# Kernel tuning notes

Measured on AMD Instinct MI355X. Metric: run time of the kernel, lower is better.

## Reference

```python
import jax, jax.numpy as jnp
import numpy as np

N_HEAD = 16

def setup_inputs() -> dict:
    key = jax.random.key(0)
    k1, k2, k3, k4, k5 = jax.random.split(key, 5)
    B, S, D = 2, 2048, 1024
    return {
        "hidden_states": jax.random.normal(k1, (B, S, D), jnp.float32),
        "w_attn": jax.random.normal(k2, (D, 3 * D), jnp.float32) * 0.02,
        "b_attn": jax.random.normal(k3, (3 * D,), jnp.float32) * 0.02,
        "w_proj": jax.random.normal(k4, (D, D), jnp.float32) * 0.02,
        "b_proj": jax.random.normal(k5, (D,), jnp.float32) * 0.02,
    }

def reference(hidden_states, w_attn, b_attn, w_proj, b_proj):
    B, S, D = hidden_states.shape
    H = N_HEAD
    Dh = D // H
    qkv = hidden_states @ w_attn + b_attn              # [B,S,3D]
    q, k, v = jnp.split(qkv, 3, axis=-1)
    def split_heads(x):
        return x.reshape(B, S, H, Dh).transpose(0, 2, 1, 3)  # [B,H,S,Dh]
    q, k, v = split_heads(q), split_heads(k), split_heads(v)
    # scale=True: divide by sqrt(head_dim) (v.size(-1))
    scores = jnp.einsum("bhqd,bhkd->bhqk", q, k) / jnp.sqrt(jnp.float32(Dh))
    attn = jax.nn.softmax(scores, axis=-1)             # [B,H,S,S]
    out = jnp.einsum("bhqk,bhkd->bhqd", attn, v)       # [B,H,S,Dh]
    out = out.transpose(0, 2, 1, 3).reshape(B, S, D)   # merge heads
    return out @ w_proj + b_proj
```

## Files before the change

kernel.cpp:

```cpp
#include <hip/hip_runtime.h>
#include <hip/hip_bf16.h>

typedef __attribute__((ext_vector_type(8))) short bf16x8;
typedef __attribute__((ext_vector_type(4))) float f32x4;
typedef __attribute__((ext_vector_type(16))) float f32x16;

#define LOG2E 1.4426950408889634f
#define SCALE_F (0.125f * LOG2E)

__device__ inline unsigned short f2bf(float f) {
  union { float f; unsigned u; } x; x.f = f;
  unsigned u = x.u;
  unsigned r = u + 0x7FFFu + ((u >> 16) & 1u);
  return (unsigned short)(r >> 16);
}

__device__ inline unsigned cvtpk(float lo, float hi) {
  unsigned r;
  asm("v_cvt_pk_bf16_f32 %0, %1, %2" : "=v"(r) : "v"(lo), "v"(hi));
  return r;
}

__device__ inline void gload16(const unsigned short* g, unsigned short* l) {
  __builtin_amdgcn_global_load_lds(
      (const __attribute__((address_space(1))) unsigned int*)g,
      (__attribute__((address_space(3))) unsigned int*)l, 16, 0, 0);
}

template <int J>
__device__ inline bf16x8 pack_pfrag(f32x16 p) {
  int X, Y, Z, W;
  asm("v_cvt_pk_bf16_f32 %0, %1, %2" : "=v"(X) : "v"(p[J + 0]), "v"(p[J + 1]));
  asm("v_cvt_pk_bf16_f32 %0, %1, %2" : "=v"(Y) : "v"(p[J + 2]), "v"(p[J + 3]));
  asm("v_cvt_pk_bf16_f32 %0, %1, %2" : "=v"(Z) : "v"(p[J + 4]), "v"(p[J + 5]));
  asm("v_cvt_pk_bf16_f32 %0, %1, %2" : "=v"(W) : "v"(p[J + 6]), "v"(p[J + 7]));
  asm("v_permlane32_swap_b32 %0, %1" : "+v"(X), "+v"(Z));
  asm("v_permlane32_swap_b32 %0, %1" : "+v"(Y), "+v"(W));
  union { int w[4]; bf16x8 v; } u;
  u.w[0] = X; u.w[1] = Y; u.w[2] = Z; u.w[3] = W;
  return u.v;
}

__global__ __launch_bounds__(256) void cvt_bf16(const float* __restrict__ X,
                                                unsigned short* __restrict__ Y, int n4) {
  int i = blockIdx.x * blockDim.x + threadIdx.x;
  int stride = gridDim.x * blockDim.x;
  for (; i < n4; i += stride) {
    float4 v = reinterpret_cast<const float4*>(X)[i];
    ushort4 o;
    o.x = f2bf(v.x); o.y = f2bf(v.y); o.z = f2bf(v.z); o.w = f2bf(v.w);
    reinterpret_cast<ushort4*>(Y)[i] = o;
  }
}

__global__ __launch_bounds__(256) void transpose_cvt(const float* __restrict__ W,
                                                     unsigned short* __restrict__ WT,
                                                     int K, int N) {
  __shared__ unsigned short Tl[64][72];
  const int t = threadIdx.x;
  const int n0 = blockIdx.x * 64, k0 = blockIdx.y * 64;
#pragma unroll
  for (int i = 0; i < 4; ++i) {
    int idx = t + i * 256;
    int r = idx >> 4, c4 = (idx & 15) << 2;
    float4 v = *reinterpret_cast<const float4*>(&W[(size_t)(k0 + r) * N + n0 + c4]);
    Tl[c4 + 0][r] = f2bf(v.x);
    Tl[c4 + 1][r] = f2bf(v.y);
    Tl[c4 + 2][r] = f2bf(v.z);
    Tl[c4 + 3][r] = f2bf(v.w);
  }
  __syncthreads();
#pragma unroll
  for (int i = 0; i < 2; ++i) {
    int idx = t + i * 256;
    int rr = idx >> 3, cc = (idx & 7) << 3;
    *reinterpret_cast<int4*>(&WT[(size_t)(n0 + rr) * K + k0 + cc]) =
        *reinterpret_cast<const int4*>(&Tl[rr][cc]);
  }
}

__global__ __launch_bounds__(512, 2) void gemm_qkv_8p(
    const unsigned short* __restrict__ A, const unsigned short* __restrict__ Bt,
    const float* __restrict__ bias,
    unsigned short* __restrict__ qw, unsigned short* __restrict__ kw,
    unsigned short* __restrict__ vtg) {
  __shared__ unsigned short Abuf[2][16384];
  __shared__ unsigned short Bbuf[2][12288];
  const int t = threadIdx.x, lane = t & 63, wid = t >> 6;
  const int wm = wid >> 2, wn = wid & 3;
  const int orig = blockIdx.x;
  const int nid = (orig & 7) * 32 + (orig >> 3);
  const int mt = nid >> 4, nt = nid & 15;
  const int row0 = mt * 256, col0 = nt * 192;
  const int lr = lane & 15, kq = lane >> 4;
  const int srow_lo = lane >> 3;
  const int scg = (lane & 7) ^ srow_lo;
  const unsigned short* Ab = A + (size_t)row0 * 1024;
  const unsigned short* Bb = Bt + (size_t)col0 * 1024;
  f32x4 acc[8][3] = {};

#define SA8(bs, kt)                                                              \
  {                                                                              \
    const unsigned short* Ap = Ab + (kt) * 64;                                   \
    _Pragma("unroll") for (int i = 0; i < 4; ++i) {                              \
      int g = wid * 4 + i;                                                       \
      int rrel = g * 8 + srow_lo;                                                \
      gload16(&Ap[(size_t)rrel * 1024 + scg * 8], &Abuf[bs][g * 512]);           \
    }                                                                            \
  }
#define SB8(bs, kt)                                                              \
  {                                                                              \
    const unsigned short* Bp = Bb + (kt) * 64;                                   \
    _Pragma("unroll") for (int i = 0; i < 3; ++i) {                              \
      int g = wid * 3 + i;                                                       \
      int rrel = g * 8 + srow_lo;                                                \
      gload16(&Bp[(size_t)rrel * 1024 + scg * 8], &Bbuf[bs][g * 512]);           \
    }                                                                            \
  }
#define RDA(dst, mh)                                                             \
  _Pragma("unroll") for (int m = 0; m < 4; ++m)                                  \
  _Pragma("unroll") for (int ks = 0; ks < 2; ++ks) {                             \
    int row = wm * 128 + (mh) * 64 + m * 16 + lr;                                \
    dst[m][ks] = *reinterpret_cast<const bf16x8*>(                               \
        &Ac[row * 64 + (((ks * 4 + kq) ^ (row & 7)) << 3)]);                     \
  }
#define RDB2(dst)                                                                \
  _Pragma("unroll") for (int n = 0; n < 2; ++n)                                  \
  _Pragma("unroll") for (int ks = 0; ks < 2; ++ks) {                             \
    int row = wn * 48 + n * 16 + lr;                                             \
    dst[n][ks] = *reinterpret_cast<const bf16x8*>(                               \
        &Bc[row * 64 + (((ks * 4 + kq) ^ (row & 7)) << 3)]);                     \
  }
#define RDB1(dst)                                                                \
  _Pragma("unroll") for (int ks = 0; ks < 2; ++ks) {                             \
    int row = wn * 48 + 32 + lr;                                                 \
    dst[0][ks] = *reinterpret_cast<const bf16x8*>(                               \
        &Bc[row * 64 + (((ks * 4 + kq) ^ (row & 7)) << 3)]);                     \
  }
#define QMM2(mh, afv, bfv)                                                       \
  _Pragma("unroll") for (int m = 0; m < 4; ++m)                                  \
  _Pragma("unroll") for (int n = 0; n < 2; ++n)                                  \
  _Pragma("unroll") for (int ks = 0; ks < 2; ++ks)                               \
    acc[(mh) * 4 + m][n] = __builtin_amdgcn_mfma_f32_16x16x32_bf16(              \
        afv[m][ks], bfv[n][ks], acc[(mh) * 4 + m][n], 0, 0, 0);
#define QMM1(mh, afv, bfv)                                                       \
  _Pragma("unroll") for (int m = 0; m < 4; ++m)                                  \
  _Pragma("unroll") for (int ks = 0; ks < 2; ++ks)                               \
    acc[(mh) * 4 + m][2] = __builtin_amdgcn_mfma_f32_16x16x32_bf16(              \
        afv[m][ks], bfv[0][ks], acc[(mh) * 4 + m][2], 0, 0, 0);
#define BAR8 __builtin_amdgcn_s_barrier();

  SA8(0, 0) SB8(0, 0)
  asm volatile("s_waitcnt vmcnt(0)" ::: "memory");
  BAR8
  __builtin_amdgcn_sched_barrier(0);

  for (int kt = 0; kt < 16; ++kt) {
    const int buf = kt & 1;
    const unsigned short* Ac = Abuf[buf];
    const unsigned short* Bc = Bbuf[buf];
    bf16x8 af0[4][2], af1[4][2], bf0[2][2], bf1[1][2];
    RDA(af0, 0) RDB2(bf0)
    if (kt < 15) SA8(buf ^ 1, kt + 1)
    BAR8
    __builtin_amdgcn_s_setprio(1); QMM2(0, af0, bf0) __builtin_amdgcn_s_setprio(0);
    BAR8
    RDA(af1, 1)
    if (kt < 15) SB8(buf ^ 1, kt + 1)
    BAR8
    __builtin_amdgcn_s_setprio(1); QMM2(1, af1, bf0) __builtin_amdgcn_s_setprio(0);
    BAR8
    RDB1(bf1)
    BAR8
    __builtin_amdgcn_s_setprio(1); QMM1(0, af0, bf1) __builtin_amdgcn_s_setprio(0);
    BAR8
    if (kt < 15) { asm volatile("s_waitcnt vmcnt(0)" ::: "memory"); }
    BAR8
    __builtin_amdgcn_s_setprio(1); QMM1(1, af1, bf1) __builtin_amdgcn_s_setprio(0);
    BAR8
    __builtin_amdgcn_sched_barrier(0);
  }
#undef SA8
#undef SB8
#undef RDA
#undef RDB2
#undef RDB1
#undef QMM2
#undef QMM1
#undef BAR8

  const int rbase = (lane >> 4) * 4;
#pragma unroll
  for (int mm = 0; mm < 8; ++mm) {
#pragma unroll
    for (int nn = 0; nn < 3; ++nn) {
      int c = col0 + wn * 48 + nn * 16 + lr;
      int which = c >> 10;
      int d = c & 1023;
      int h = d >> 6, dh = d & 63;
      float bv = bias[c];
      int m0 = row0 + wm * 128 + mm * 16 + rbase;
      int b = m0 >> 11, s0 = m0 & 2047;
      if (which == 2) {
        int kt = s0 >> 6, key0 = s0 & 63;
        ushort4 pv;
        pv.x = f2bf(acc[mm][nn][0] + bv);
        pv.y = f2bf(acc[mm][nn][1] + bv);
        pv.z = f2bf(acc[mm][nn][2] + bv);
        pv.w = f2bf(acc[mm][nn][3] + bv);
        *reinterpret_cast<ushort4*>(
            &vtg[(((size_t)(b * 16 + h) * 32 + kt) * 64 + dh) * 64 + key0]) = pv;
      } else if (which == 1) {
#pragma unroll
        for (int r = 0; r < 4; ++r)
          kw[(((size_t)b * 16 + h) * 2048 + (s0 + r)) * 64 + dh] = f2bf(acc[mm][nn][r] + bv);
      } else {
#pragma unroll
        for (int r = 0; r < 4; ++r)
          qw[(((size_t)b * 16 + h) * 2048 + (s0 + r)) * 64 + dh] =
              f2bf((acc[mm][nn][r] + bv) * SCALE_F);
      }
    }
  }
}

#define GST(bs, kt)                                                             \
  {                                                                             \
    const unsigned short* Ap = Ab + (kt) * 32;                                  \
    const unsigned short* Bp = Bb + (kt) * 32;                                  \
    _Pragma("unroll") for (int i = 0; i < 2; ++i) {                             \
      int row = i * 64 + wid * 16 + s_r;                                        \
      gload16(&Ap[(size_t)row * 1024 + s_c], &Al[bs][i * 2048 + wid * 512]);    \
      gload16(&Bp[(size_t)row * 1024 + s_c], &Bl[bs][i * 2048 + wid * 512]);    \
    }                                                                           \
  }

#define GBODY(br)                                                               \
  {                                                                             \
    bf16x8 af[4], bfv[4];                                                       \
    _Pragma("unroll") for (int mm = 0; mm < 4; ++mm) {                          \
      int row = wr + mm * 16 + lr;                                              \
      af[mm] = *reinterpret_cast<const bf16x8*>(                                \
          &Al[br][row * 32 + ((kq ^ (lr & 3)) << 3)]);                          \
    }                                                                           \
    _Pragma("unroll") for (int nn = 0; nn < 4; ++nn) {                          \
      int row = wc + nn * 16 + lr;                                              \
      bfv[nn] = *reinterpret_cast<const bf16x8*>(                               \
          &Bl[br][row * 32 + ((kq ^ (lr & 3)) << 3)]);                          \
    }                                                                           \
    _Pragma("unroll") for (int mm = 0; mm < 4; ++mm)                            \
      _Pragma("unroll") for (int nn = 0; nn < 4; ++nn)                          \
        acc[mm][nn] =                                                           \
            __builtin_amdgcn_mfma_f32_16x16x32_bf16(af[mm], bfv[nn],            \
                                                    acc[mm][nn], 0, 0, 0);      \
  }

#define VMC4 asm volatile("s_waitcnt vmcnt(4)" ::: "memory");
#define VMC0 asm volatile("s_waitcnt vmcnt(0)" ::: "memory");
#define BAR __builtin_amdgcn_s_barrier();

__global__ __launch_bounds__(256) void gemm_proj_b(
    const unsigned short* __restrict__ A, const unsigned short* __restrict__ Bt,
    const float* __restrict__ bias, float* __restrict__ out) {
  const int N = 1024;
  __shared__ unsigned short Al[3][4096];
  __shared__ unsigned short Bl[3][4096];
  const int t = threadIdx.x, lane = t & 63, wid = t >> 6;
  const int wr = (wid >> 1) * 64, wc = (wid & 1) * 64;
  const int orig = blockIdx.x + 8 * blockIdx.y;
  const int nid = (orig & 7) * 32 + (orig >> 3);
  const int row0 = (nid >> 3) * 128, col0 = (nid & 7) * 128;
  const int lr = lane & 15, kq = lane >> 4;
  const int s_r = lane >> 2;
  const int s_c = ((lane & 3) ^ (s_r & 3)) * 8;
  const unsigned short* Ab = A + (size_t)row0 * 1024;
  const unsigned short* Bb = Bt + (size_t)col0 * 1024;
  f32x4 acc[4][4] = {};

  GST(0, 0) GST(1, 1)
  VMC4 BAR
  for (int tt = 0; tt < 30; tt += 3) {
    GST(2, tt + 2) GBODY(0) VMC4 BAR
    GST(0, tt + 3) GBODY(1) VMC4 BAR
    GST(1, tt + 4) GBODY(2) VMC4 BAR
  }
  GBODY(0) VMC0 BAR
  GBODY(1)

  const int rbase = (lane >> 4) * 4;
#pragma unroll
  for (int mm = 0; mm < 4; ++mm) {
#pragma unroll
    for (int nn = 0; nn < 4; ++nn) {
      int c = col0 + wc + nn * 16 + lr;
      float bv = bias[c];
#pragma unroll
      for (int r = 0; r < 4; ++r) {
        int m = row0 + wr + mm * 16 + rbase + r;
        out[(size_t)m * N + c] = acc[mm][nn][r] + bv;
      }
    }
  }
}

__global__ __launch_bounds__(512, 4) void attn_kernel(
    const unsigned short* __restrict__ qw, const unsigned short* __restrict__ kw,
    const unsigned short* __restrict__ vtg, unsigned short* __restrict__ ow) {
  __shared__ char smem[65536];
  unsigned short* KV = (unsigned short*)smem;
  unsigned short* Ol = (unsigned short*)smem;
  float* EX = (float*)(smem + 18432);
  const int t = threadIdx.x, lane = t & 63, wid = t >> 6;
  const int half = wid >> 2, wq = wid & 3;
  const int l31 = lane & 31, hi = lane >> 5;
  const int orig = blockIdx.x + 16 * blockIdx.y;
  const int nid = (orig & 7) * 64 + (orig >> 3);
  const int qt = nid & 15, bh = nid >> 4;
  const int b = bh >> 4, h = bh & 15;
  const unsigned short* Qg = qw + (size_t)bh * 2048 * 64;
  const unsigned short* Kg = kw + (size_t)bh * 2048 * 64;
  const unsigned short* Vg = vtg + (size_t)bh * 32 * 4096;
  const int q0 = qt * 128 + wq * 32;

  union { short s[8]; bf16x8 v; } one_u;
#pragma unroll
  for (int i = 0; i < 8; ++i) one_u.s[i] = (short)0x3F80;
  const bf16x8 ones = one_u.v;

  bf16x8 qf[4];
#pragma unroll
  for (int kc = 0; kc < 4; ++kc)
    qf[kc] = *reinterpret_cast<const bf16x8*>(&Qg[(q0 + l31) * 64 + kc * 16 + hi * 8]);

  f32x16 oA = {0,0,0,0,0,0,0,0,0,0,0,0,0,0,0,0};
  f32x16 oB = {0,0,0,0,0,0,0,0,0,0,0,0,0,0,0,0};
  f32x16 lC = {0,0,0,0,0,0,0,0,0,0,0,0,0,0,0,0};

  const int srow_lo = lane >> 3;
  const int scg = (lane & 7) ^ srow_lo;

#define STAGE(buf, kt)                                                              \
  {                                                                                 \
    const unsigned short* Kt = Kg + (size_t)(kt) * 4096;                            \
    const unsigned short* Vs = Vg + (size_t)(kt) * 4096;                            \
    unsigned short* Kl = KV + half * 16384 + (buf) * 8192;                          \
    unsigned short* Vl = Kl + 4096;                                                 \
    _Pragma("unroll") for (int i = 0; i < 2; ++i) {                                 \
      int chunk = wq * 2 + i;                                                       \
      int row = chunk * 8 + srow_lo;                                                \
      gload16(&Kt[row * 64 + scg * 8], &Kl[chunk * 512]);                           \
      gload16(&Vs[row * 64 + scg * 8], &Vl[chunk * 512]);                           \
    }                                                                               \
  }

  const int kt0 = half * 16;
  STAGE(0, kt0)

  for (int it = 0; it < 16; ++it) {
    const int cur = it & 1;
    if (it + 1 < 16) {
      STAGE(cur ^ 1, kt0 + it + 1)
      asm volatile("s_waitcnt vmcnt(4)" ::: "memory");
    } else {
      asm volatile("s_waitcnt vmcnt(0)" ::: "memory");
    }
    __builtin_amdgcn_s_barrier();
    const unsigned short* Kl = KV + half * 16384 + cur * 8192;
    const unsigned short* Vl = Kl + 4096;

    f32x16 sA = {0,0,0,0,0,0,0,0,0,0,0,0,0,0,0,0};
    f32x16 sB = {0,0,0,0,0,0,0,0,0,0,0,0,0,0,0,0};
    __builtin_amdgcn_s_setprio(1);
#pragma unroll
    for (int kc = 0; kc < 4; ++kc) {
      bf16x8 k0f = *reinterpret_cast<const bf16x8*>(
          &Kl[l31 * 64 + (((kc * 2 + hi) ^ (l31 & 7)) << 3)]);
      bf16x8 k1f = *reinterpret_cast<const bf16x8*>(
          &Kl[(32 + l31) * 64 + (((kc * 2 + hi) ^ (l31 & 7)) << 3)]);
      sA = __builtin_amdgcn_mfma_f32_32x32x16_bf16(k0f, qf[kc], sA, 0, 0, 0);
      sB = __builtin_amdgcn_mfma_f32_32x32x16_bf16(k1f, qf[kc], sB, 0, 0, 0);
    }
    __builtin_amdgcn_s_setprio(0);

#pragma unroll
    for (int j = 0; j < 16; ++j) {
      sA[j] = exp2f(sA[j]);
      sB[j] = exp2f(sB[j]);
    }

    bf16x8 pf0 = pack_pfrag<0>(sA);
    bf16x8 pf1 = pack_pfrag<8>(sA);
    bf16x8 pf2 = pack_pfrag<0>(sB);
    bf16x8 pf3 = pack_pfrag<8>(sB);

    __builtin_amdgcn_s_setprio(1);
#pragma unroll
    for (int c = 0; c < 4; ++c) {
      bf16x8 pf = (c == 0) ? pf0 : (c == 1) ? pf1 : (c == 2) ? pf2 : pf3;
      int g = c * 2 + hi;
      bf16x8 v0f = *reinterpret_cast<const bf16x8*>(
          &Vl[l31 * 64 + ((g ^ (l31 & 7)) << 3)]);
      bf16x8 v1f = *reinterpret_cast<const bf16x8*>(
          &Vl[(32 + l31) * 64 + ((g ^ (l31 & 7)) << 3)]);
      oA = __builtin_amdgcn_mfma_f32_32x32x16_bf16(v0f, pf, oA, 0, 0, 0);
      oB = __builtin_amdgcn_mfma_f32_32x32x16_bf16(v1f, pf, oB, 0, 0, 0);
      lC = __builtin_amdgcn_mfma_f32_32x32x16_bf16(ones, pf, lC, 0, 0, 0);
    }
    __builtin_amdgcn_s_setprio(0);
    __builtin_amdgcn_s_barrier();
  }
#undef STAGE

  __syncthreads();
  if (half == 1) {
    float* e = EX + ((size_t)(wq * 64 + lane)) * 34;
#pragma unroll
    for (int j = 0; j < 16; ++j) { e[j] = oA[j]; e[16 + j] = oB[j]; }
    e[32] = lC[0];
  }
  __syncthreads();
  if (half == 0) {
    const float* e = EX + ((size_t)(wq * 64 + lane)) * 34;
    float linv = 1.0f / (lC[0] + e[32]);
    unsigned short* orow_l = Ol + (wq * 32 + l31) * 72;
#pragma unroll
    for (int g = 0; g < 4; ++g) {
      float a0 = (oA[4 * g + 0] + e[4 * g + 0]) * linv;
      float a1v = (oA[4 * g + 1] + e[4 * g + 1]) * linv;
      float a2v = (oA[4 * g + 2] + e[4 * g + 2]) * linv;
      float a3v = (oA[4 * g + 3] + e[4 * g + 3]) * linv;
      uint2 w0; w0.x = cvtpk(a0, a1v); w0.y = cvtpk(a2v, a3v);
      *reinterpret_cast<uint2*>(&orow_l[8 * g + 4 * hi]) = w0;
      float b0 = (oB[4 * g + 0] + e[16 + 4 * g + 0]) * linv;
      float b1v = (oB[4 * g + 1] + e[16 + 4 * g + 1]) * linv;
      float b2v = (oB[4 * g + 2] + e[16 + 4 * g + 2]) * linv;
      float b3v = (oB[4 * g + 3] + e[16 + 4 * g + 3]) * linv;
      uint2 w1; w1.x = cvtpk(b0, b1v); w1.y = cvtpk(b2v, b3v);
      *reinterpret_cast<uint2*>(&orow_l[32 + 8 * g + 4 * hi]) = w1;
    }
  }
  __syncthreads();
#pragma unroll
  for (int i = 0; i < 2; ++i) {
    int idx = t + i * 512;
    int q = idx >> 3, ch = idx & 7;
    int4 v = *reinterpret_cast<const int4*>(&Ol[q * 72 + ch * 8]);
    *reinterpret_cast<int4*>(
        &ow[(((size_t)b * 2048 + qt * 128 + q) * 16 + h) * 64 + ch * 8]) = v;
  }
}

extern "C" void kernel_launch(void* const* d_in, const int* in_sizes, int n_in,
                              void* d_out, int out_size, void* d_ws, size_t ws_size,
                              hipStream_t stream) {
  const float* hs = (const float*)d_in[0];
  const float* w_attn = (const float*)d_in[1];
  const float* b_attn = (const float*)d_in[2];
  const float* w_proj = (const float*)d_in[3];
  const float* b_proj = (const float*)d_in[4];
  float* out = (float*)d_out;

  const size_t HEAD = (size_t)2 * 16 * 2048 * 64;
  unsigned short* qw = (unsigned short*)d_ws;
  unsigned short* kw = qw + HEAD;
  unsigned short* vtg = kw + HEAD;
  unsigned short* hs_b = vtg + HEAD;
  unsigned short* ow = hs_b;
  unsigned short* wT = hs_b + HEAD;
  unsigned short* pT = wT + (size_t)3072 * 1024;

  cvt_bf16<<<2048, 256, 0, stream>>>(hs, hs_b, 1048576);
  transpose_cvt<<<dim3(48, 16), 256, 0, stream>>>(w_attn, wT, 1024, 3072);
  transpose_cvt<<<dim3(16, 16), 256, 0, stream>>>(w_proj, pT, 1024, 1024);

  gemm_qkv_8p<<<dim3(256), 512, 0, stream>>>(hs_b, wT, b_attn, qw, kw, vtg);
  attn_kernel<<<dim3(16, 32), 512, 0, stream>>>(qw, kw, vtg, ow);
  gemm_proj_b<<<dim3(8, 32), 256, 0, stream>>>(ow, pT, b_proj, out);
}
```

Baseline: 125.1 us.

## Fuse prep kernels, replace ones-MFMA row sum, and reswizzle attention LDS

```diff
diff --git a/kernel.cpp b/kernel.cpp
--- a/kernel.cpp
+++ b/kernel.cpp
@@ -41,24 +41,10 @@
   return u.v;
 }
 
-__global__ __launch_bounds__(256) void cvt_bf16(const float* __restrict__ X,
-                                                unsigned short* __restrict__ Y, int n4) {
-  int i = blockIdx.x * blockDim.x + threadIdx.x;
-  int stride = gridDim.x * blockDim.x;
-  for (; i < n4; i += stride) {
-    float4 v = reinterpret_cast<const float4*>(X)[i];
-    ushort4 o;
-    o.x = f2bf(v.x); o.y = f2bf(v.y); o.z = f2bf(v.z); o.w = f2bf(v.w);
-    reinterpret_cast<ushort4*>(Y)[i] = o;
-  }
-}
-
-__global__ __launch_bounds__(256) void transpose_cvt(const float* __restrict__ W,
-                                                     unsigned short* __restrict__ WT,
-                                                     int K, int N) {
-  __shared__ unsigned short Tl[64][72];
-  const int t = threadIdx.x;
-  const int n0 = blockIdx.x * 64, k0 = blockIdx.y * 64;
+__device__ inline void transpose_tile(const float* __restrict__ W,
+                                      unsigned short* __restrict__ WT, int K, int N,
+                                      int n0, int k0, int t,
+                                      unsigned short (*Tl)[72]) {
 #pragma unroll
   for (int i = 0; i < 4; ++i) {
     int idx = t + i * 256;
@@ -76,6 +62,30 @@
     int rr = idx >> 3, cc = (idx & 7) << 3;
     *reinterpret_cast<int4*>(&WT[(size_t)(n0 + rr) * K + k0 + cc]) =
         *reinterpret_cast<const int4*>(&Tl[rr][cc]);
+  }
+}
+
+__global__ __launch_bounds__(256) void prep_fused(
+    const float* __restrict__ hs, unsigned short* __restrict__ hs_b,
+    const float* __restrict__ w_attn, unsigned short* __restrict__ wT,
+    const float* __restrict__ w_proj, unsigned short* __restrict__ pT) {
+  __shared__ unsigned short Tl[64][72];
+  const int bid = blockIdx.x, t = threadIdx.x;
+  if (bid < 768) {
+    transpose_tile(w_attn, wT, 1024, 3072, (bid % 48) * 64, (bid / 48) * 64, t, Tl);
+  } else if (bid < 1024) {
+    int r = bid - 768;
+    transpose_tile(w_proj, pT, 1024, 1024, (r % 16) * 64, (r / 16) * 64, t, Tl);
+  } else {
+    int cb = bid - 1024;
+#pragma unroll
+    for (int j = 0; j < 4; ++j) {
+      int i = cb * 1024 + j * 256 + t;
+      float4 v = reinterpret_cast<const float4*>(hs)[i];
+      ushort4 o;
+      o.x = f2bf(v.x); o.y = f2bf(v.y); o.z = f2bf(v.z); o.w = f2bf(v.w);
+      reinterpret_cast<ushort4*>(hs_b)[i] = o;
+    }
   }
 }
 
@@ -322,11 +332,6 @@
   const unsigned short* Vg = vtg + (size_t)bh * 32 * 4096;
   const int q0 = qt * 128 + wq * 32;
 
-  union { short s[8]; bf16x8 v; } one_u;
-#pragma unroll
-  for (int i = 0; i < 8; ++i) one_u.s[i] = (short)0x3F80;
-  const bf16x8 ones = one_u.v;
-
   bf16x8 qf[4];
 #pragma unroll
   for (int kc = 0; kc < 4; ++kc)
@@ -334,10 +339,11 @@
 
   f32x16 oA = {0,0,0,0,0,0,0,0,0,0,0,0,0,0,0,0};
   f32x16 oB = {0,0,0,0,0,0,0,0,0,0,0,0,0,0,0,0};
-  f32x16 lC = {0,0,0,0,0,0,0,0,0,0,0,0,0,0,0,0};
+  float lrun = 0.f;
 
   const int srow_lo = lane >> 3;
-  const int scg = (lane & 7) ^ srow_lo;
+  const int scg0 = (lane & 7) ^ srow_lo;
+  const int rsw = (l31 & 7) ^ ((l31 >> 3) & 3);
 
 #define STAGE(buf, kt)                                                              \
   {                                                                                 \
@@ -348,8 +354,9 @@
     _Pragma("unroll") for (int i = 0; i < 2; ++i) {                                 \
       int chunk = wq * 2 + i;                                                       \
       int row = chunk * 8 + srow_lo;                                                \
-      gload16(&Kt[row * 64 + scg * 8], &Kl[chunk * 512]);                           \
-      gload16(&Vs[row * 64 + scg * 8], &Vl[chunk * 512]);                           \
+      int sc = (scg0 ^ (chunk & 3)) * 8;                                            \
+      gload16(&Kt[row * 64 + sc], &Kl[chunk * 512]);                                \
+      gload16(&Vs[row * 64 + sc], &Vl[chunk * 512]);                                \
     }                                                                               \
   }
 
@@ -374,19 +381,27 @@
 #pragma unroll
     for (int kc = 0; kc < 4; ++kc) {
       bf16x8 k0f = *reinterpret_cast<const bf16x8*>(
-          &Kl[l31 * 64 + (((kc * 2 + hi) ^ (l31 & 7)) << 3)]);
+          &Kl[l31 * 64 + (((kc * 2 + hi) ^ rsw) << 3)]);
       bf16x8 k1f = *reinterpret_cast<const bf16x8*>(
-          &Kl[(32 + l31) * 64 + (((kc * 2 + hi) ^ (l31 & 7)) << 3)]);
+          &Kl[(32 + l31) * 64 + (((kc * 2 + hi) ^ rsw) << 3)]);
       sA = __builtin_amdgcn_mfma_f32_32x32x16_bf16(k0f, qf[kc], sA, 0, 0, 0);
       sB = __builtin_amdgcn_mfma_f32_32x32x16_bf16(k1f, qf[kc], sB, 0, 0, 0);
     }
     __builtin_amdgcn_s_setprio(0);
 
+    float rsv[16];
 #pragma unroll
     for (int j = 0; j < 16; ++j) {
-      sA[j] = exp2f(sA[j]);
-      sB[j] = exp2f(sB[j]);
-    }
+      float pa = exp2f(sA[j]);
+      float pb = exp2f(sB[j]);
+      sA[j] = pa; sB[j] = pb;
+      rsv[j] = pa + pb;
+    }
+#pragma unroll
+    for (int s = 8; s >= 1; s >>= 1)
+#pragma unroll
+      for (int j = 0; j < s; ++j) rsv[j] += rsv[j + s];
+    lrun += rsv[0] + __shfl_xor(rsv[0], 32);
 
     bf16x8 pf0 = pack_pfrag<0>(sA);
     bf16x8 pf1 = pack_pfrag<8>(sA);
@@ -399,12 +414,11 @@
       bf16x8 pf = (c == 0) ? pf0 : (c == 1) ? pf1 : (c == 2) ? pf2 : pf3;
       int g = c * 2 + hi;
       bf16x8 v0f = *reinterpret_cast<const bf16x8*>(
-          &Vl[l31 * 64 + ((g ^ (l31 & 7)) << 3)]);
+          &Vl[l31 * 64 + ((g ^ rsw) << 3)]);
       bf16x8 v1f = *reinterpret_cast<const bf16x8*>(
-          &Vl[(32 + l31) * 64 + ((g ^ (l31 & 7)) << 3)]);
+          &Vl[(32 + l31) * 64 + ((g ^ rsw) << 3)]);
       oA = __builtin_amdgcn_mfma_f32_32x32x16_bf16(v0f, pf, oA, 0, 0, 0);
       oB = __builtin_amdgcn_mfma_f32_32x32x16_bf16(v1f, pf, oB, 0, 0, 0);
-      lC = __builtin_amdgcn_mfma_f32_32x32x16_bf16(ones, pf, lC, 0, 0, 0);
     }
     __builtin_amdgcn_s_setprio(0);
     __builtin_amdgcn_s_barrier();
@@ -416,12 +430,12 @@
     float* e = EX + ((size_t)(wq * 64 + lane)) * 34;
 #pragma unroll
     for (int j = 0; j < 16; ++j) { e[j] = oA[j]; e[16 + j] = oB[j]; }
-    e[32] = lC[0];
+    e[32] = lrun;
   }
   __syncthreads();
   if (half == 0) {
     const float* e = EX + ((size_t)(wq * 64 + lane)) * 34;
-    float linv = 1.0f / (lC[0] + e[32]);
+    float linv = 1.0f / (lrun + e[32]);
     unsigned short* orow_l = Ol + (wq * 32 + l31) * 72;
 #pragma unroll
     for (int g = 0; g < 4; ++g) {
@@ -469,9 +483,7 @@
   unsigned short* wT = hs_b + HEAD;
   unsigned short* pT = wT + (size_t)3072 * 1024;
 
-  cvt_bf16<<<2048, 256, 0, stream>>>(hs, hs_b, 1048576);
-  transpose_cvt<<<dim3(48, 16), 256, 0, stream>>>(w_attn, wT, 1024, 3072);
-  transpose_cvt<<<dim3(16, 16), 256, 0, stream>>>(w_proj, pT, 1024, 1024);
+  prep_fused<<<dim3(2048), 256, 0, stream>>>(hs, hs_b, w_attn, wT, w_proj, pT);
 
   gemm_qkv_8p<<<dim3(256), 512, 0, stream>>>(hs_b, wT, b_attn, qw, kw, vtg);
   attn_kernel<<<dim3(16, 32), 512, 0, stream>>>(qw, kw, vtg, ow);
```

New measurement: 118.9 us. 1.05x faster.
